# Kernel tuning notes

Hardware: AMD Instinct MI355X
Metric: run time of the kernel (lower is better)

Reference implementation:

```python
import jax, jax.numpy as jnp
from jax import lax
import numpy as np

IN_C, OUT_C, K, N_SPLIT = 256, 256, 3, 4
N_LEGO = int(OUT_C * 0.25)          # 64
BASIC_C = IN_C // N_SPLIT           # 64


def setup_inputs() -> dict:
    key = jax.random.key(0)
    k1, k2, k3, k4 = jax.random.split(key, 4)
    x = jax.random.normal(k1, (32, IN_C, 56, 56), dtype=jnp.float32)
    # kaiming-normal-ish initialization of parameters
    lego = jax.random.normal(k2, (N_LEGO, BASIC_C, K, 1), dtype=jnp.float32) * np.sqrt(2.0 / (BASIC_C * K))
    aux_coefficients = jax.random.normal(k3, (N_SPLIT, OUT_C, N_LEGO, 1, 1), dtype=jnp.float32) * np.sqrt(2.0 / N_LEGO)
    aux_combination = jax.random.normal(k4, (N_SPLIT, OUT_C, N_LEGO, 1, 1), dtype=jnp.float32) * np.sqrt(2.0 / N_LEGO)
    return {"x": x, "lego": lego, "aux_coefficients": aux_coefficients, "aux_combination": aux_combination}


def reference(x, lego, aux_coefficients, aux_combination):
    n_split, out_c, n_lego = aux_combination.shape[:3]
    bc = lego.shape[1]
    # one-hot selection: each (split, out_channel) picks exactly one lego feature
    idx = jnp.argmax(aux_combination[..., 0, 0], axis=2)              # (n_split, out_c)
    proxy = jax.nn.one_hot(idx, n_lego, dtype=x.dtype)                # (n_split, out_c, n_lego)
    W = aux_coefficients[..., 0, 0] * proxy                           # (n_split, out_c, n_lego)
    out = 0.0
    for i in range(n_split):
        xi = x[:, i * bc:(i + 1) * bc]                                # (B, bc, H, W)
        feat = lax.conv_general_dilated(
            xi, lego, window_strides=(3, 1), padding=((1, 1), (1, 1)),
            dimension_numbers=("NCHW", "OIHW", "NCHW"))               # (B, n_lego, Ho, Wo)
        out = out + jnp.einsum("bnhw,on->bohw", feat, W[i])
    return out
```

## Files before the change

### kernel.cpp

```cpp
#include <hip/hip_runtime.h>

#define INC    256
#define HIN    56
#define WIN    56
#define HOUT   19
#define WOUT   58
#define HW     3136

typedef short frag8 __attribute__((ext_vector_type(8)));
typedef float f32x4 __attribute__((ext_vector_type(4)));
typedef float f4    __attribute__((ext_vector_type(4)));

static __device__ __forceinline__ unsigned short f2bf(float f) {
    unsigned u = __float_as_uint(f);
    u += 0x7fffu + ((u >> 16) & 1u);
    return (unsigned short)(u >> 16);
}

static __device__ __forceinline__ unsigned cvtpk(float a, float b) {
    unsigned r;
    asm("v_cvt_pk_bf16_f32 %0, %1, %2" : "=v"(r) : "v"(a), "v"(b));
    return r;
}

#define VMCNT(n) asm volatile("s_waitcnt vmcnt(" #n ")" ::: "memory")
#define FENCE()  asm volatile("" ::: "memory")

__global__ __launch_bounds__(256) void prep_weff(
    const float* __restrict__ lego,
    const float* __restrict__ coefs,
    const float* __restrict__ comb,
    unsigned short* __restrict__ Asw)
{
    __shared__ int   idxS[4];
    __shared__ float cofS[4];
    const int t  = threadIdx.x;
    const int kx = blockIdx.x;
    const int o  = blockIdx.y;
    const int wv = t >> 6, l = t & 63;

    float v  = comb[(wv * 256 + o) * 64 + l];
    int   bi = l;
    #pragma unroll
    for (int off = 32; off >= 1; off >>= 1) {
        float ov = __shfl_xor(v, off, 64);
        int   oi = __shfl_xor(bi, off, 64);
        if (ov > v || (ov == v && oi < bi)) { v = ov; bi = oi; }
    }
    if (l == 0) {
        idxS[wv] = bi;
        cofS[wv] = coefs[(wv * 256 + o) * 64 + bi];
    }
    __syncthreads();

    const int k  = kx * 256 + t;
    const int kh = k >> 8, c = k & 255;
    const int i  = c >> 6, cl = c & 63;
    float w = cofS[i] * lego[idxS[i] * 192 + cl * 3 + kh];

    const int o_tile = o >> 4, m = o & 15;
    const int ks = k >> 5, kc = (k >> 3) & 3, j = k & 7;
    Asw[((((size_t)o_tile * 24 + ks) * 64) + kc * 16 + m) * 8 + j] = f2bf(w);
}

__global__ __launch_bounds__(256, 3) void conv_mfma(
    const float* __restrict__ x,
    const unsigned short* __restrict__ Asw,
    float* __restrict__ out)
{
    __shared__ float Xs[3][4096];

    const int t  = threadIdx.x;
    const int h  = blockIdx.x;
    const int b  = blockIdx.y;
    const int l  = t & 63;
    const int lo = l & 15;
    const int hi = l >> 4;
    const int wv = t >> 6;
    const int kc = hi;

    int slotb[4];
    #pragma unroll
    for (int wt = 0; wt < 4; ++wt) {
        int c    = wt * 16 + lo;
        int slot = (c & 32) | ((c + 8 * kc) & 31);
        slotb[wt] = slot * 4;
    }
    const int bko = kc * 2048;

    const int gs = l & 15, chof = l >> 4;
    unsigned goff[4];
    int      ldsu[4];
    #pragma unroll
    for (int i = 0; i < 4; ++i) {
        int I    = wv * 4 + i;
        int chl  = I * 4 + chof;
        int kcs  = (chl >> 3) & 3;
        int half = gs >> 3, gsw = gs & 7;
        int g    = (gsw - 2 * kcs) & 7;
        int col  = half * 32 + g * 4;
        if (col >= WIN) col = 0;
        goff[i] = (unsigned)chl * HW + col;
        ldsu[i] = I * 1024;
    }

    const float* xb = x + (size_t)b * (INC * HW);
    const frag8* Af = (const frag8*)Asw + (size_t)(wv * 4) * 24 * 64 + l;
    char* XsB = (char*)&Xs[0][0];

    f32x4 acc[4][4];
    #pragma unroll
    for (int ot = 0; ot < 4; ++ot)
        #pragma unroll
        for (int wt = 0; wt < 4; ++wt)
            acc[ot][wt] = (f32x4){0.f, 0.f, 0.f, 0.f};

    auto STAGE = [&](int q) {
        const int kh = q >> 2, cq = q & 3;
        const int row = 3 * h - 1 + kh;
        const int bufo = (q % 3) * 16384;
        if (row < 0) {
            f4 z = (f4){0.f, 0.f, 0.f, 0.f};
            #pragma unroll
            for (int i = 0; i < 4; ++i)
                *(f4*)(XsB + bufo + ldsu[i] + l * 16) = z;
            asm volatile("s_waitcnt lgkmcnt(0)" ::: "memory");
        } else {
            const float* rp = xb + (size_t)cq * 64 * HW + row * WIN;
            #pragma unroll
            for (int i = 0; i < 4; ++i) {
                __builtin_amdgcn_global_load_lds(
                    (const __attribute__((address_space(1))) void*)(rp + goff[i]),
                    (__attribute__((address_space(3))) void*)(XsB + bufo + ldsu[i]),
                    16, 0, 0);
            }
        }
    };

    STAGE(0);
    STAGE(1);

    #pragma unroll
    for (int q = 0; q < 12; ++q) {
        if (q + 2 < 12) STAGE(q + 2);

        frag8 a[4][2];
        #pragma unroll
        for (int ot = 0; ot < 4; ++ot)
            #pragma unroll
            for (int ksl = 0; ksl < 2; ++ksl)
                a[ot][ksl] = Af[(ot * 24 + q * 2 + ksl) * 64];

        if (q < 10)       { VMCNT(16); }
        else if (q == 10) { VMCNT(12); }
        else              { VMCNT(8);  }
        __builtin_amdgcn_s_barrier();
        FENCE();

        const char* bb = XsB + (q % 3) * 16384 + bko;
        #pragma unroll
        for (int ksl = 0; ksl < 2; ++ksl) {
            #pragma unroll
            for (int wt = 0; wt < 4; ++wt) {
                float f0 = *(const float*)(bb + ksl * 8192 + 0 * 256 + slotb[wt]);
                float f1 = *(const float*)(bb + ksl * 8192 + 1 * 256 + slotb[wt]);
                float f2 = *(const float*)(bb + ksl * 8192 + 2 * 256 + slotb[wt]);
                float f3 = *(const float*)(bb + ksl * 8192 + 3 * 256 + slotb[wt]);
                float f4_ = *(const float*)(bb + ksl * 8192 + 4 * 256 + slotb[wt]);
                float f5 = *(const float*)(bb + ksl * 8192 + 5 * 256 + slotb[wt]);
                float f6 = *(const float*)(bb + ksl * 8192 + 6 * 256 + slotb[wt]);
                float f7 = *(const float*)(bb + ksl * 8192 + 7 * 256 + slotb[wt]);
                union { frag8 fr; unsigned u[4]; } B;
                B.u[0] = cvtpk(f0, f1);
                B.u[1] = cvtpk(f2, f3);
                B.u[2] = cvtpk(f4_, f5);
                B.u[3] = cvtpk(f6, f7);
                #pragma unroll
                for (int ot = 0; ot < 4; ++ot)
                    acc[ot][wt] = __builtin_amdgcn_mfma_f32_16x16x32_bf16(
                        a[ot][ksl], B.fr, acc[ot][wt], 0, 0, 0);
            }
        }
        FENCE();
        __builtin_amdgcn_s_barrier();
    }

    #pragma unroll
    for (int ot = 0; ot < 4; ++ot) {
        #pragma unroll
        for (int r = 0; r < 4; ++r) {
            int o = wv * 64 + ot * 16 + hi * 4 + r;
            float* orow = out + ((size_t)(b * 256 + o) * HOUT + h) * WOUT;
            #pragma unroll
            for (int wt = 0; wt < 4; ++wt) {
                int n = wt * 16 + lo;
                if (n < 56) orow[n + 1] = acc[ot][wt][r];
            }
            if (lo == 0) orow[0]  = 0.f;
            if (lo == 1) orow[57] = 0.f;
        }
    }
}

extern "C" void kernel_launch(void* const* d_in, const int* in_sizes, int n_in,
                              void* d_out, int out_size, void* d_ws, size_t ws_size,
                              hipStream_t stream) {
    const float* x     = (const float*)d_in[0];
    const float* lego  = (const float*)d_in[1];
    const float* coefs = (const float*)d_in[2];
    const float* comb  = (const float*)d_in[3];
    float* out = (float*)d_out;

    unsigned short* Asw = (unsigned short*)d_ws;

    prep_weff<<<dim3(3, 256), 256, 0, stream>>>(lego, coefs, comb, Asw);
    conv_mfma<<<dim3(HOUT, 32), 256, 0, stream>>>(x, Asw, out);
}
```

Before: 193.8 us.

## Prefetch weight fragments one stage ahead and retune LDS swizzle

Weight fragments for stage q+1 now load into a double-buffered register array during stage q, rather than right before use. This hides global load latency behind the MFMA work. The LDS swizzle offset changes from 8*kc to 16*kc, with a matching change to the global column rotation, to alter the bank-conflict pattern. vmcnt waits are adjusted to account for the extra in-flight loads, and the last stage waits for everything. The cost is more live registers, which may reduce occupancy below the target of 3 blocks.

```diff
diff --git a/kernel.cpp b/kernel.cpp
--- a/kernel.cpp
+++ b/kernel.cpp
@@ -83,7 +83,7 @@
     #pragma unroll
     for (int wt = 0; wt < 4; ++wt) {
         int c    = wt * 16 + lo;
-        int slot = (c & 32) | ((c + 8 * kc) & 31);
+        int slot = (c & 32) | ((c + 16 * kc) & 31);
         slotb[wt] = slot * 4;
     }
     const int bko = kc * 2048;
@@ -97,7 +97,7 @@
         int chl  = I * 4 + chof;
         int kcs  = (chl >> 3) & 3;
         int half = gs >> 3, gsw = gs & 7;
-        int g    = (gsw - 2 * kcs) & 7;
+        int g    = (gsw - 4 * kcs) & 7;
         int col  = half * 32 + g * 4;
         if (col >= WIN) col = 0;
         goff[i] = (unsigned)chl * HW + col;
@@ -137,23 +137,31 @@
         }
     };
 
+    frag8 A2[2][4][2];
+    #pragma unroll
+    for (int ot = 0; ot < 4; ++ot)
+        #pragma unroll
+        for (int ksl = 0; ksl < 2; ++ksl)
+            A2[0][ot][ksl] = Af[(ot * 24 + 0 * 2 + ksl) * 64];
+    __builtin_amdgcn_sched_barrier(0);
     STAGE(0);
     STAGE(1);
 
     #pragma unroll
     for (int q = 0; q < 12; ++q) {
+        if (q + 1 < 12) {
+            #pragma unroll
+            for (int ot = 0; ot < 4; ++ot)
+                #pragma unroll
+                for (int ksl = 0; ksl < 2; ++ksl)
+                    A2[(q + 1) & 1][ot][ksl] = Af[(ot * 24 + (q + 1) * 2 + ksl) * 64];
+        }
+        __builtin_amdgcn_sched_barrier(0);
         if (q + 2 < 12) STAGE(q + 2);
-
-        frag8 a[4][2];
-        #pragma unroll
-        for (int ot = 0; ot < 4; ++ot)
-            #pragma unroll
-            for (int ksl = 0; ksl < 2; ++ksl)
-                a[ot][ksl] = Af[(ot * 24 + q * 2 + ksl) * 64];
 
         if (q < 10)       { VMCNT(16); }
         else if (q == 10) { VMCNT(12); }
-        else              { VMCNT(8);  }
+        else              { VMCNT(0);  }
         __builtin_amdgcn_s_barrier();
         FENCE();
 
@@ -162,14 +170,15 @@
         for (int ksl = 0; ksl < 2; ++ksl) {
             #pragma unroll
             for (int wt = 0; wt < 4; ++wt) {
-                float f0 = *(const float*)(bb + ksl * 8192 + 0 * 256 + slotb[wt]);
-                float f1 = *(const float*)(bb + ksl * 8192 + 1 * 256 + slotb[wt]);
-                float f2 = *(const float*)(bb + ksl * 8192 + 2 * 256 + slotb[wt]);
-                float f3 = *(const float*)(bb + ksl * 8192 + 3 * 256 + slotb[wt]);
-                float f4_ = *(const float*)(bb + ksl * 8192 + 4 * 256 + slotb[wt]);
-                float f5 = *(const float*)(bb + ksl * 8192 + 5 * 256 + slotb[wt]);
-                float f6 = *(const float*)(bb + ksl * 8192 + 6 * 256 + slotb[wt]);
-                float f7 = *(const float*)(bb + ksl * 8192 + 7 * 256 + slotb[wt]);
+                const char* p0 = bb + ksl * 8192 + slotb[wt];
+                float f0 = *(const float*)(p0 + 0 * 256);
+                float f1 = *(const float*)(p0 + 1 * 256);
+                float f2 = *(const float*)(p0 + 2 * 256);
+                float f3 = *(const float*)(p0 + 3 * 256);
+                float f4_ = *(const float*)(p0 + 4 * 256);
+                float f5 = *(const float*)(p0 + 5 * 256);
+                float f6 = *(const float*)(p0 + 6 * 256);
+                float f7 = *(const float*)(p0 + 7 * 256);
                 union { frag8 fr; unsigned u[4]; } B;
                 B.u[0] = cvtpk(f0, f1);
                 B.u[1] = cvtpk(f2, f3);
@@ -178,7 +187,7 @@
                 #pragma unroll
                 for (int ot = 0; ot < 4; ++ot)
                     acc[ot][wt] = __builtin_amdgcn_mfma_f32_16x16x32_bf16(
-                        a[ot][ksl], B.fr, acc[ot][wt], 0, 0, 0);
+                        A2[q & 1][ot][ksl], B.fr, acc[ot][wt], 0, 0, 0);
             }
         }
         FENCE();
```

After: 240.0 us. 1.24x slower.

## Stage activations through registers, convert to bf16 before LDS, double-buffer

Applied to the files above, without the earlier changes.

Replaces the direct global-to-LDS fp32 staging with per-thread register loads that are converted to bf16 and written to LDS already in MFMA fragment layout, so the inner loop reads a single 16-byte fragment instead of eight scalar floats plus conversions. The weight buffer is reordered so each K-step's A fragments are contiguous. The pipeline becomes a two-buffer register-to-LDS scheme with explicit sched barriers and wait counts. This halves the LDS footprint and the LDS reads, but adds VGPR pressure (16 floats plus fragments) and puts conversion and LDS writes onto the critical path between barriers.

```diff
diff --git a/kernel.cpp b/kernel.cpp
--- a/kernel.cpp
+++ b/kernel.cpp
@@ -9,7 +9,6 @@
 
 typedef short frag8 __attribute__((ext_vector_type(8)));
 typedef float f32x4 __attribute__((ext_vector_type(4)));
-typedef float f4    __attribute__((ext_vector_type(4)));
 
 static __device__ __forceinline__ unsigned short f2bf(float f) {
     unsigned u = __float_as_uint(f);
@@ -24,7 +23,9 @@
 }
 
 #define VMCNT(n) asm volatile("s_waitcnt vmcnt(" #n ")" ::: "memory")
+#define LGKM0()  asm volatile("s_waitcnt lgkmcnt(0)" ::: "memory")
 #define FENCE()  asm volatile("" ::: "memory")
+#define SB0()    __builtin_amdgcn_sched_barrier(0)
 
 __global__ __launch_bounds__(256) void prep_weff(
     const float* __restrict__ lego,
@@ -60,7 +61,8 @@
 
     const int o_tile = o >> 4, m = o & 15;
     const int ks = k >> 5, kc = (k >> 3) & 3, j = k & 7;
-    Asw[((((size_t)o_tile * 24 + ks) * 64) + kc * 16 + m) * 8 + j] = f2bf(w);
+    const int ks2 = ks >> 1, ksl = ks & 1;
+    Asw[((((size_t)ks2 * 16 + o_tile) * 2 + ksl) * 64 + kc * 16 + m) * 8 + j] = f2bf(w);
 }
 
 __global__ __launch_bounds__(256, 3) void conv_mfma(
@@ -68,7 +70,7 @@
     const unsigned short* __restrict__ Asw,
     float* __restrict__ out)
 {
-    __shared__ float Xs[3][4096];
+    __shared__ unsigned short Xs[2][4096];
 
     const int t  = threadIdx.x;
     const int h  = blockIdx.x;
@@ -77,36 +79,28 @@
     const int lo = l & 15;
     const int hi = l >> 4;
     const int wv = t >> 6;
-    const int kc = hi;
-
-    int slotb[4];
-    #pragma unroll
-    for (int wt = 0; wt < 4; ++wt) {
-        int c    = wt * 16 + lo;
-        int slot = (c & 32) | ((c + 8 * kc) & 31);
-        slotb[wt] = slot * 4;
-    }
-    const int bko = kc * 2048;
-
-    const int gs = l & 15, chof = l >> 4;
-    unsigned goff[4];
-    int      ldsu[4];
-    #pragma unroll
-    for (int i = 0; i < 4; ++i) {
-        int I    = wv * 4 + i;
-        int chl  = I * 4 + chof;
-        int kcs  = (chl >> 3) & 3;
-        int half = gs >> 3, gsw = gs & 7;
-        int g    = (gsw - 2 * kcs) & 7;
-        int col  = half * 32 + g * 4;
-        if (col >= WIN) col = 0;
-        goff[i] = (unsigned)chl * HW + col;
-        ldsu[i] = I * 1024;
-    }
+
+    const int cw   = t & 31;
+    const int kg   = (t >> 5) & 7;
+    const int kslw = kg >> 2, kcw = kg & 3;
+    const int c1u  = cw + 32;
+    const int c1   = (c1u < WIN) ? c1u : (WIN - 1);
+    int voff[16];
+    #pragma unroll
+    for (int j = 0; j < 8; ++j) {
+        voff[j]     = (kg * 8 + j) * HW + cw;
+        voff[8 + j] = (kg * 8 + j) * HW + c1;
+    }
+    const int ws0 = (kslw * 4 + (cw  >> 4)) * 64 + kcw * 16 + (cw  & 15);
+    const int ws1 = (kslw * 4 + (c1u >> 4)) * 64 + kcw * 16 + (c1u & 15);
+    unsigned short* Wp[2][2];
+    Wp[0][0] = &Xs[0][ws0 * 8];  Wp[0][1] = &Xs[0][ws1 * 8];
+    Wp[1][0] = &Xs[1][ws0 * 8];  Wp[1][1] = &Xs[1][ws1 * 8];
 
     const float* xb = x + (size_t)b * (INC * HW);
-    const frag8* Af = (const frag8*)Asw + (size_t)(wv * 4) * 24 * 64 + l;
-    char* XsB = (char*)&Xs[0][0];
+    const frag8* Afw = (const frag8*)Asw + l;
+    const frag8* Xf[2] = { (const frag8*)&Xs[0][0] + l,
+                           (const frag8*)&Xs[1][0] + l };
 
     f32x4 acc[4][4];
     #pragma unroll
@@ -115,74 +109,81 @@
         for (int wt = 0; wt < 4; ++wt)
             acc[ot][wt] = (f32x4){0.f, 0.f, 0.f, 0.f};
 
-    auto STAGE = [&](int q) {
-        const int kh = q >> 2, cq = q & 3;
+    frag8 A[4][2];
+    float Lv[16];
+
+    auto LOADL = [&](int q) {
+        const int kh  = q >> 2, cq = q & 3;
         const int row = 3 * h - 1 + kh;
-        const int bufo = (q % 3) * 16384;
-        if (row < 0) {
-            f4 z = (f4){0.f, 0.f, 0.f, 0.f};
-            #pragma unroll
-            for (int i = 0; i < 4; ++i)
-                *(f4*)(XsB + bufo + ldsu[i] + l * 16) = z;
-            asm volatile("s_waitcnt lgkmcnt(0)" ::: "memory");
-        } else {
-            const float* rp = xb + (size_t)cq * 64 * HW + row * WIN;
-            #pragma unroll
-            for (int i = 0; i < 4; ++i) {
-                __builtin_amdgcn_global_load_lds(
-                    (const __attribute__((address_space(1))) void*)(rp + goff[i]),
-                    (__attribute__((address_space(3))) void*)(XsB + bufo + ldsu[i]),
-                    16, 0, 0);
-            }
-        }
+        const int rc  = row < 0 ? 0 : row;
+        const float zmask = row < 0 ? 0.f : 1.f;
+        const float* xq = xb + (size_t)cq * 64 * HW + (size_t)rc * WIN;
+        #pragma unroll
+        for (int i = 0; i < 16; ++i) Lv[i] = xq[voff[i]] * zmask;
     };
 
-    STAGE(0);
-    STAGE(1);
-
-    #pragma unroll
-    for (int q = 0; q < 12; ++q) {
-        if (q + 2 < 12) STAGE(q + 2);
-
-        frag8 a[4][2];
+    auto LOADA = [&](int q) {
         #pragma unroll
         for (int ot = 0; ot < 4; ++ot)
             #pragma unroll
             for (int ksl = 0; ksl < 2; ++ksl)
-                a[ot][ksl] = Af[(ot * 24 + q * 2 + ksl) * 64];
-
-        if (q < 10)       { VMCNT(16); }
-        else if (q == 10) { VMCNT(12); }
-        else              { VMCNT(8);  }
-        __builtin_amdgcn_s_barrier();
-        FENCE();
-
-        const char* bb = XsB + (q % 3) * 16384 + bko;
+                A[ot][ksl] = Afw[q * 2048 + wv * 512 + ot * 128 + ksl * 64];
+    };
+
+    auto W = [&](int q) {
+        const int bp = q & 1;
+        union { frag8 fr; unsigned u[4]; } P;
+        P.u[0] = cvtpk(Lv[0], Lv[1]);
+        P.u[1] = cvtpk(Lv[2], Lv[3]);
+        P.u[2] = cvtpk(Lv[4], Lv[5]);
+        P.u[3] = cvtpk(Lv[6], Lv[7]);
+        *(frag8*)Wp[bp][0] = P.fr;
+        P.u[0] = cvtpk(Lv[8],  Lv[9]);
+        P.u[1] = cvtpk(Lv[10], Lv[11]);
+        P.u[2] = cvtpk(Lv[12], Lv[13]);
+        P.u[3] = cvtpk(Lv[14], Lv[15]);
+        *(frag8*)Wp[bp][1] = P.fr;
+    };
+
+    LOADA(0);
+    SB0();
+    LOADL(0);
+    SB0();
+    VMCNT(0);
+    W(0);
+    LOADL(1);
+    SB0();
+    LGKM0();
+    __builtin_amdgcn_s_barrier();
+    FENCE();
+
+    #pragma unroll
+    for (int q = 0; q < 12; ++q) {
+        const int bp = q & 1;
         #pragma unroll
         for (int ksl = 0; ksl < 2; ++ksl) {
             #pragma unroll
             for (int wt = 0; wt < 4; ++wt) {
-                float f0 = *(const float*)(bb + ksl * 8192 + 0 * 256 + slotb[wt]);
-                float f1 = *(const float*)(bb + ksl * 8192 + 1 * 256 + slotb[wt]);
-                float f2 = *(const float*)(bb + ksl * 8192 + 2 * 256 + slotb[wt]);
-                float f3 = *(const float*)(bb + ksl * 8192 + 3 * 256 + slotb[wt]);
-                float f4_ = *(const float*)(bb + ksl * 8192 + 4 * 256 + slotb[wt]);
-                float f5 = *(const float*)(bb + ksl * 8192 + 5 * 256 + slotb[wt]);
-                float f6 = *(const float*)(bb + ksl * 8192 + 6 * 256 + slotb[wt]);
-                float f7 = *(const float*)(bb + ksl * 8192 + 7 * 256 + slotb[wt]);
-                union { frag8 fr; unsigned u[4]; } B;
-                B.u[0] = cvtpk(f0, f1);
-                B.u[1] = cvtpk(f2, f3);
-                B.u[2] = cvtpk(f4_, f5);
-                B.u[3] = cvtpk(f6, f7);
+                frag8 B = Xf[bp][(ksl * 4 + wt) * 64];
                 #pragma unroll
                 for (int ot = 0; ot < 4; ++ot)
                     acc[ot][wt] = __builtin_amdgcn_mfma_f32_16x16x32_bf16(
-                        a[ot][ksl], B.fr, acc[ot][wt], 0, 0, 0);
+                        A[ot][ksl], B, acc[ot][wt], 0, 0, 0);
             }
         }
-        FENCE();
-        __builtin_amdgcn_s_barrier();
+
+        if (q < 11) {
+            SB0();
+            LOADA(q + 1);
+            SB0();
+            VMCNT(8);
+            W(q + 1);
+            if (q < 10) LOADL(q + 2);
+            SB0();
+            LGKM0();
+            __builtin_amdgcn_s_barrier();
+            FENCE();
+        }
     }
 
     #pragma unroll
```

Result: no change. 197.0 us (+1.6%).
